# Kernel tuning notes

Measured on AMD Instinct MI355X. Metric: run time of the kernel, lower is better.

## Reference

```python
import jax, jax.numpy as jnp
import numpy as np

H = 32  # hidden_size

def _lstm_layer(x, Wih, Whh, bih, bhh):
    """Single LSTM layer, batch_first x: [B,T,I] -> hs [B,T,H].
    PyTorch gate order: i, f, g, o."""
    B = x.shape[0]
    # Precompute all input projections at once: [B,T,4H] -> time-major [T,B,4H]
    xp = (jnp.einsum('bti,gi->btg', x, Wih) + bih + bhh).transpose(1, 0, 2)
    h0 = jnp.zeros((B, H), dtype=x.dtype)
    c0 = jnp.zeros((B, H), dtype=x.dtype)

    def step(carry, xt):
        h, c = carry
        gates = xt + h @ Whh.T                      # [B,4H]
        i, f, g, o = jnp.split(gates, 4, axis=-1)
        i = jax.nn.sigmoid(i)
        f = jax.nn.sigmoid(f)
        g = jnp.tanh(g)
        o = jax.nn.sigmoid(o)
        c = f * c + i * g
        h = o * jnp.tanh(c)
        return (h, c), h

    _, hs = jax.lax.scan(step, (h0, c0), xp)        # hs: [T,B,H]
    return hs.transpose(1, 0, 2)                    # [B,T,H]


def setup_inputs() -> dict:
    key = jax.random.key(0)
    ks = jax.random.split(key, 12)
    B, T, I = 4096, 512, 1
    s = 1.0 / np.sqrt(H)  # PyTorch uniform(-1/sqrt(H), 1/sqrt(H)) init scale
    u = lambda k, shape: jax.random.uniform(k, shape, jnp.float32, -s, s)
    return {
        'x': jax.random.normal(ks[0], (B, T, I), jnp.float32),
        'W_ih_l0': u(ks[1], (4 * H, I)),
        'W_hh_l0': u(ks[2], (4 * H, H)),
        'b_ih_l0': u(ks[3], (4 * H,)),
        'b_hh_l0': u(ks[4], (4 * H,)),
        'W_ih_l1': u(ks[5], (4 * H, H)),
        'W_hh_l1': u(ks[6], (4 * H, H)),
        'b_ih_l1': u(ks[7], (4 * H,)),
        'b_hh_l1': u(ks[8], (4 * H,)),
        'W_fc': u(ks[9], (1, H)),
        'b_fc': u(ks[10], (1,)),
    }


def reference(x, W_ih_l0, W_hh_l0, b_ih_l0, b_hh_l0,
              W_ih_l1, W_hh_l1, b_ih_l1, b_hh_l1, W_fc, b_fc):
    h1 = _lstm_layer(x, W_ih_l0, W_hh_l0, b_ih_l0, b_hh_l0)   # [B,T,H]
    h2 = _lstm_layer(h1, W_ih_l1, W_hh_l1, b_ih_l1, b_hh_l1)  # [B,T,H]
    out = h2[:, -1, :] @ W_fc.T + b_fc                        # [B,1]
    return jax.nn.relu(out)
```

## Files before the change

kernel.cpp:

```cpp
#include <hip/hip_runtime.h>
#include <hip/hip_bf16.h>


typedef __attribute__((ext_vector_type(8))) short bf16x8;
typedef __attribute__((ext_vector_type(4))) float f32x4;
typedef __attribute__((ext_vector_type(4))) int   i32x4;

#define HID 32
#define SEQ 512
#define L2E 1.4426950408889634f
#define LSTR 20

static __device__ __forceinline__ float fexp2(float x){ return __builtin_amdgcn_exp2f(x); }
static __device__ __forceinline__ float frcp (float x){ return __builtin_amdgcn_rcpf(x); }
static __device__ __forceinline__ short f2bf(float f){
  unsigned u = __builtin_bit_cast(unsigned, f);
  u = (u + 0x7fffu + ((u >> 16) & 1u)) >> 16;
  return (short)u;
}

#define CELL(gi, gf, gg, go, cvr, hout) do {                         \
  const float I_ = fexp2(gi), G_ = fexp2(gg);                        \
  const float F_ = fexp2(gf), O_ = fexp2(go);                        \
  const float a_ = 1.f + I_, b_ = 1.f + G_, c_ = 1.f + F_;           \
  const float P1_ = a_ * b_;                                         \
  const float R_  = frcp(c_ * P1_);                                  \
  const float fv_ = P1_ * R_;                                        \
  const float ig_ = (G_ - 1.f) * (c_ * R_);                          \
  (cvr) = fmaf(fv_, (cvr), ig_);                                     \
  const float C2_ = fexp2((cvr) * (2.f * L2E));                      \
  (hout) = (C2_ - 1.f) * frcp((1.f + O_) * (1.f + C2_));             \
} while (0)

#define HPACK(hv, pk) do {                                                    \
  const int pa_ = __builtin_amdgcn_ds_swizzle(__builtin_bit_cast(int, (hv)), 0x401F); \
  asm("v_cvt_pk_bf16_f32 %0, %1, %2" : "=v"(pk)                               \
      : "v"(hv), "v"(__builtin_bit_cast(float, pa_)));                        \
} while (0)

__global__ __launch_bounds__(512, 2) void lstm2_zs_kernel(
    const float* __restrict__ x,
    const float* __restrict__ Wih0, const float* __restrict__ Whh0,
    const float* __restrict__ bih0, const float* __restrict__ bhh0,
    const float* __restrict__ Wih1, const float* __restrict__ Whh1,
    const float* __restrict__ bih1, const float* __restrict__ bhh1,
    const float* __restrict__ Wfc, const float* __restrict__ bfc,
    float* __restrict__ out)
{
  const int tid = threadIdx.x;
  const int w   = tid >> 6;
  const int l   = tid & 63;
  const int m   = l >> 4;
  const int col = l & 15;
  const int V   = w & 3;
  const bool isL1 = (w >= 4);

  __shared__ int   bufH0[2][16 * LSTR];
  __shared__ int   bufH1[2][16 * LSTR];
  __shared__ float bufFC[4][16];

  for (int i = tid; i < 2 * 16 * LSTR; i += 512) {
    ((int*)bufH0)[i] = 0;
    ((int*)bufH1)[i] = 0;
  }
  __syncthreads();

  const float* Wrec = isL1 ? Whh1 : Whh0;
  const float* Bi   = isL1 ? bih1 : bih0;
  const float* Bh   = isL1 ? bhh1 : bhh0;
  const int   gcol  = col & 3;
  const float scA   = (gcol == 2) ? (2.0f * L2E) : (-L2E);
  bf16x8 wfR[2], wfI[2];
  f32x4  cb[2];
  float  w0x[2][4];
  #pragma unroll
  for (int t = 0; t < 2; ++t) {
    const int ur = 8 * V + 4 * t + (col >> 2);
    const int ga = gcol * 32 + ur;
    #pragma unroll
    for (int j = 0; j < 8; ++j) {
      wfR[t][j] = f2bf(scA * Wrec[ga * HID + (8 * m + j)]);
      wfI[t][j] = isL1 ? f2bf(scA * Wih1[ga * HID + (8 * m + j)]) : (short)0;
    }
    const int uc = 8 * V + 4 * t + m;
    #pragma unroll
    for (int rr = 0; rr < 4; ++rr) {
      const float sc = (rr == 2) ? (2.0f * L2E) : (-L2E);
      cb[t][rr] = sc * (Bi[rr * 32 + uc] + Bh[rr * 32 + uc]);
      w0x[t][rr] = isL1 ? 0.f : sc * Wih0[rr * 32 + uc];
    }
  }
  const float wfcA = isL1 ? Wfc[8 * V + m]     : 0.f;
  const float wfcB = isL1 ? Wfc[8 * V + 4 + m] : 0.f;

  float cvA = 0.f, cvB = 0.f, hA = 0.f, hB = 0.f;
  const float* xb = x + (size_t)(blockIdx.x * 16 + col) * SEQ;
  const int  rd = col * LSTR + 4 * m;
  const int  wb = col * LSTR + 4 * V + (m >> 1);
  const bool wr = ((m & 1) == 0);

  for (int k = 0; k < SEQ / 4; ++k) {
    float4 xv = {0.f, 0.f, 0.f, 0.f};
    if (!isL1) xv = *reinterpret_cast<const float4*>(xb + k * 4);
    #pragma unroll
    for (int uu = 0; uu < 4; ++uu) {
      const int par = uu & 1;
      if (!isL1) {
        const i32x4 hv = *(const i32x4*)&bufH0[par ^ 1][rd];
        const bf16x8 hf = __builtin_bit_cast(bf16x8, hv);
        f32x4 A0, A1;
        A0 = __builtin_amdgcn_mfma_f32_16x16x32_bf16(wfR[0], hf, cb[0], 0, 0, 0);
        A1 = __builtin_amdgcn_mfma_f32_16x16x32_bf16(wfR[1], hf, cb[1], 0, 0, 0);
        const float xt = (uu == 0) ? xv.x : (uu == 1) ? xv.y : (uu == 2) ? xv.z : xv.w;
        CELL(fmaf(w0x[0][0], xt, A0[0]), fmaf(w0x[0][1], xt, A0[1]),
             fmaf(w0x[0][2], xt, A0[2]), fmaf(w0x[0][3], xt, A0[3]), cvA, hA);
        CELL(fmaf(w0x[1][0], xt, A1[0]), fmaf(w0x[1][1], xt, A1[1]),
             fmaf(w0x[1][2], xt, A1[2]), fmaf(w0x[1][3], xt, A1[3]), cvB, hB);
        int pkA, pkB;
        HPACK(hA, pkA);
        HPACK(hB, pkB);
        if (wr) { bufH0[par][wb] = pkA; bufH0[par][wb + 2] = pkB; }
      } else if (uu > 0 || k > 0) {
        const i32x4 h0v = *(const i32x4*)&bufH0[par ^ 1][rd];
        const i32x4 h1v = *(const i32x4*)&bufH1[par][rd];
        const bf16x8 h0f = __builtin_bit_cast(bf16x8, h0v);
        const bf16x8 h1f = __builtin_bit_cast(bf16x8, h1v);
        f32x4 A0, A1;
        __builtin_amdgcn_s_setprio(1);
        A0 = __builtin_amdgcn_mfma_f32_16x16x32_bf16(wfI[0], h0f, cb[0], 0, 0, 0);
        A1 = __builtin_amdgcn_mfma_f32_16x16x32_bf16(wfI[1], h0f, cb[1], 0, 0, 0);
        A0 = __builtin_amdgcn_mfma_f32_16x16x32_bf16(wfR[0], h1f, A0, 0, 0, 0);
        A1 = __builtin_amdgcn_mfma_f32_16x16x32_bf16(wfR[1], h1f, A1, 0, 0, 0);
        __builtin_amdgcn_s_setprio(0);
        CELL(A0[0], A0[1], A0[2], A0[3], cvA, hA);
        CELL(A1[0], A1[1], A1[2], A1[3], cvB, hB);
        int pkA, pkB;
        HPACK(hA, pkA);
        HPACK(hB, pkB);
        if (wr) { bufH1[par ^ 1][wb] = pkA; bufH1[par ^ 1][wb + 2] = pkB; }
      }
      __syncthreads();
    }
  }

  if (isL1) {
    const i32x4 h0v = *(const i32x4*)&bufH0[1][rd];
    const i32x4 h1v = *(const i32x4*)&bufH1[0][rd];
    const bf16x8 h0f = __builtin_bit_cast(bf16x8, h0v);
    const bf16x8 h1f = __builtin_bit_cast(bf16x8, h1v);
    f32x4 A0, A1;
    A0 = __builtin_amdgcn_mfma_f32_16x16x32_bf16(wfI[0], h0f, cb[0], 0, 0, 0);
    A1 = __builtin_amdgcn_mfma_f32_16x16x32_bf16(wfI[1], h0f, cb[1], 0, 0, 0);
    A0 = __builtin_amdgcn_mfma_f32_16x16x32_bf16(wfR[0], h1f, A0, 0, 0, 0);
    A1 = __builtin_amdgcn_mfma_f32_16x16x32_bf16(wfR[1], h1f, A1, 0, 0, 0);
    CELL(A0[0], A0[1], A0[2], A0[3], cvA, hA);
    CELL(A1[0], A1[1], A1[2], A1[3], cvB, hB);
    float part = hA * wfcA + hB * wfcB;
    part += __shfl_xor(part, 16);
    part += __shfl_xor(part, 32);
    if (l < 16) bufFC[V][l] = part;
  }
  __syncthreads();
  if (w == 4 && l < 16) {
    const float o = bufFC[0][l] + bufFC[1][l] + bufFC[2][l] + bufFC[3][l] + bfc[0];
    out[blockIdx.x * 16 + l] = o > 0.f ? o : 0.f;
  }
}

extern "C" void kernel_launch(void* const* d_in, const int* in_sizes, int n_in,
                              void* d_out, int out_size, void* d_ws, size_t ws_size,
                              hipStream_t stream) {
  const float* x    = (const float*)d_in[0];
  const float* Wih0 = (const float*)d_in[1];
  const float* Whh0 = (const float*)d_in[2];
  const float* bih0 = (const float*)d_in[3];
  const float* bhh0 = (const float*)d_in[4];
  const float* Wih1 = (const float*)d_in[5];
  const float* Whh1 = (const float*)d_in[6];
  const float* bih1 = (const float*)d_in[7];
  const float* bhh1 = (const float*)d_in[8];
  const float* Wfc  = (const float*)d_in[9];
  const float* bfc  = (const float*)d_in[10];

  const int B = 4096;
  const int grid = B / 16;
  lstm2_zs_kernel<<<grid, 512, 0, stream>>>(
      x, Wih0, Whh0, bih0, bhh0, Wih1, Whh1, bih1, bhh1, Wfc, bfc,
      (float*)d_out);
}
```

Measured before the change: 197.7 us.

## Split each LSTM layer across eight waves with one hidden-unit slice each

Doubles the block to 1024 threads so each layer uses eight waves, each handling four hidden units (one MFMA tile) instead of two tiles per wave. This halves the per-wave serial work per timestep (MFMAs, cell math, packing) on the recurrence critical path. In exchange every timestep barrier now synchronises 16 waves instead of 8, and occupancy per CU changes with the larger blocks.

Result: slower. 209.3 us (+5.9%).

```diff
diff --git a/kernel.cpp b/kernel.cpp
--- a/kernel.cpp
+++ b/kernel.cpp
@@ -38,7 +38,7 @@
       : "v"(hv), "v"(__builtin_bit_cast(float, pa_)));                        \
 } while (0)
 
-__global__ __launch_bounds__(512, 2) void lstm2_zs_kernel(
+__global__ __launch_bounds__(1024, 4) void lstm2_zs16_kernel(
     const float* __restrict__ x,
     const float* __restrict__ Wih0, const float* __restrict__ Whh0,
     const float* __restrict__ bih0, const float* __restrict__ bhh0,
@@ -52,16 +52,17 @@
   const int l   = tid & 63;
   const int m   = l >> 4;
   const int col = l & 15;
-  const int V   = w & 3;
-  const bool isL1 = (w >= 4);
+  const int V   = w & 7;
+  const bool isL1 = (w >= 8);
+  const int unit = 4 * V + m;
 
   __shared__ int   bufH0[2][16 * LSTR];
   __shared__ int   bufH1[2][16 * LSTR];
-  __shared__ float bufFC[4][16];
+  __shared__ float bufFC[8][16];
 
-  for (int i = tid; i < 2 * 16 * LSTR; i += 512) {
-    ((int*)bufH0)[i] = 0;
-    ((int*)bufH1)[i] = 0;
+  if (tid < 2 * 16 * LSTR) {
+    ((int*)bufH0)[tid] = 0;
+    ((int*)bufH1)[tid] = 0;
   }
   __syncthreads();
 
@@ -70,33 +71,27 @@
   const float* Bh   = isL1 ? bhh1 : bhh0;
   const int   gcol  = col & 3;
   const float scA   = (gcol == 2) ? (2.0f * L2E) : (-L2E);
-  bf16x8 wfR[2], wfI[2];
-  f32x4  cb[2];
-  float  w0x[2][4];
+  const int   ga    = gcol * 32 + 4 * V + (col >> 2);
+  bf16x8 wfR, wfI;
+  f32x4  cb;
+  float  w0x[4];
   #pragma unroll
-  for (int t = 0; t < 2; ++t) {
-    const int ur = 8 * V + 4 * t + (col >> 2);
-    const int ga = gcol * 32 + ur;
-    #pragma unroll
-    for (int j = 0; j < 8; ++j) {
-      wfR[t][j] = f2bf(scA * Wrec[ga * HID + (8 * m + j)]);
-      wfI[t][j] = isL1 ? f2bf(scA * Wih1[ga * HID + (8 * m + j)]) : (short)0;
-    }
-    const int uc = 8 * V + 4 * t + m;
-    #pragma unroll
-    for (int rr = 0; rr < 4; ++rr) {
-      const float sc = (rr == 2) ? (2.0f * L2E) : (-L2E);
-      cb[t][rr] = sc * (Bi[rr * 32 + uc] + Bh[rr * 32 + uc]);
-      w0x[t][rr] = isL1 ? 0.f : sc * Wih0[rr * 32 + uc];
-    }
+  for (int j = 0; j < 8; ++j) {
+    wfR[j] = f2bf(scA * Wrec[ga * HID + (8 * m + j)]);
+    wfI[j] = isL1 ? f2bf(scA * Wih1[ga * HID + (8 * m + j)]) : (short)0;
   }
-  const float wfcA = isL1 ? Wfc[8 * V + m]     : 0.f;
-  const float wfcB = isL1 ? Wfc[8 * V + 4 + m] : 0.f;
+  #pragma unroll
+  for (int rr = 0; rr < 4; ++rr) {
+    const float sc = (rr == 2) ? (2.0f * L2E) : (-L2E);
+    cb[rr]  = sc * (Bi[rr * 32 + unit] + Bh[rr * 32 + unit]);
+    w0x[rr] = isL1 ? 0.f : sc * Wih0[rr * 32 + unit];
+  }
+  const float wfc = isL1 ? Wfc[unit] : 0.f;
 
-  float cvA = 0.f, cvB = 0.f, hA = 0.f, hB = 0.f;
+  float cv = 0.f, hn = 0.f;
   const float* xb = x + (size_t)(blockIdx.x * 16 + col) * SEQ;
   const int  rd = col * LSTR + 4 * m;
-  const int  wb = col * LSTR + 4 * V + (m >> 1);
+  const int  wb = col * LSTR + 2 * V + (m >> 1);
   const bool wr = ((m & 1) == 0);
 
   for (int k = 0; k < SEQ / 4; ++k) {
@@ -108,36 +103,26 @@
       if (!isL1) {
         const i32x4 hv = *(const i32x4*)&bufH0[par ^ 1][rd];
         const bf16x8 hf = __builtin_bit_cast(bf16x8, hv);
-        f32x4 A0, A1;
-        A0 = __builtin_amdgcn_mfma_f32_16x16x32_bf16(wfR[0], hf, cb[0], 0, 0, 0);
-        A1 = __builtin_amdgcn_mfma_f32_16x16x32_bf16(wfR[1], hf, cb[1], 0, 0, 0);
+        const f32x4 A = __builtin_amdgcn_mfma_f32_16x16x32_bf16(wfR, hf, cb, 0, 0, 0);
         const float xt = (uu == 0) ? xv.x : (uu == 1) ? xv.y : (uu == 2) ? xv.z : xv.w;
-        CELL(fmaf(w0x[0][0], xt, A0[0]), fmaf(w0x[0][1], xt, A0[1]),
-             fmaf(w0x[0][2], xt, A0[2]), fmaf(w0x[0][3], xt, A0[3]), cvA, hA);
-        CELL(fmaf(w0x[1][0], xt, A1[0]), fmaf(w0x[1][1], xt, A1[1]),
-             fmaf(w0x[1][2], xt, A1[2]), fmaf(w0x[1][3], xt, A1[3]), cvB, hB);
-        int pkA, pkB;
-        HPACK(hA, pkA);
-        HPACK(hB, pkB);
-        if (wr) { bufH0[par][wb] = pkA; bufH0[par][wb + 2] = pkB; }
+        CELL(fmaf(w0x[0], xt, A[0]), fmaf(w0x[1], xt, A[1]),
+             fmaf(w0x[2], xt, A[2]), fmaf(w0x[3], xt, A[3]), cv, hn);
+        int pk;
+        HPACK(hn, pk);
+        if (wr) bufH0[par][wb] = pk;
       } else if (uu > 0 || k > 0) {
         const i32x4 h0v = *(const i32x4*)&bufH0[par ^ 1][rd];
         const i32x4 h1v = *(const i32x4*)&bufH1[par][rd];
         const bf16x8 h0f = __builtin_bit_cast(bf16x8, h0v);
         const bf16x8 h1f = __builtin_bit_cast(bf16x8, h1v);
-        f32x4 A0, A1;
         __builtin_amdgcn_s_setprio(1);
-        A0 = __builtin_amdgcn_mfma_f32_16x16x32_bf16(wfI[0], h0f, cb[0], 0, 0, 0);
-        A1 = __builtin_amdgcn_mfma_f32_16x16x32_bf16(wfI[1], h0f, cb[1], 0, 0, 0);
-        A0 = __builtin_amdgcn_mfma_f32_16x16x32_bf16(wfR[0], h1f, A0, 0, 0, 0);
-        A1 = __builtin_amdgcn_mfma_f32_16x16x32_bf16(wfR[1], h1f, A1, 0, 0, 0);
+        f32x4 A = __builtin_amdgcn_mfma_f32_16x16x32_bf16(wfI, h0f, cb, 0, 0, 0);
+        A = __builtin_amdgcn_mfma_f32_16x16x32_bf16(wfR, h1f, A, 0, 0, 0);
         __builtin_amdgcn_s_setprio(0);
-        CELL(A0[0], A0[1], A0[2], A0[3], cvA, hA);
-        CELL(A1[0], A1[1], A1[2], A1[3], cvB, hB);
-        int pkA, pkB;
-        HPACK(hA, pkA);
-        HPACK(hB, pkB);
-        if (wr) { bufH1[par ^ 1][wb] = pkA; bufH1[par ^ 1][wb + 2] = pkB; }
+        CELL(A[0], A[1], A[2], A[3], cv, hn);
+        int pk;
+        HPACK(hn, pk);
+        if (wr) bufH1[par ^ 1][wb] = pk;
       }
       __syncthreads();
     }
@@ -148,21 +133,19 @@
     const i32x4 h1v = *(const i32x4*)&bufH1[0][rd];
     const bf16x8 h0f = __builtin_bit_cast(bf16x8, h0v);
     const bf16x8 h1f = __builtin_bit_cast(bf16x8, h1v);
-    f32x4 A0, A1;
-    A0 = __builtin_amdgcn_mfma_f32_16x16x32_bf16(wfI[0], h0f, cb[0], 0, 0, 0);
-    A1 = __builtin_amdgcn_mfma_f32_16x16x32_bf16(wfI[1], h0f, cb[1], 0, 0, 0);
-    A0 = __builtin_amdgcn_mfma_f32_16x16x32_bf16(wfR[0], h1f, A0, 0, 0, 0);
-    A1 = __builtin_amdgcn_mfma_f32_16x16x32_bf16(wfR[1], h1f, A1, 0, 0, 0);
-    CELL(A0[0], A0[1], A0[2], A0[3], cvA, hA);
-    CELL(A1[0], A1[1], A1[2], A1[3], cvB, hB);
-    float part = hA * wfcA + hB * wfcB;
+    f32x4 A = __builtin_amdgcn_mfma_f32_16x16x32_bf16(wfI, h0f, cb, 0, 0, 0);
+    A = __builtin_amdgcn_mfma_f32_16x16x32_bf16(wfR, h1f, A, 0, 0, 0);
+    CELL(A[0], A[1], A[2], A[3], cv, hn);
+    float part = hn * wfc;
     part += __shfl_xor(part, 16);
     part += __shfl_xor(part, 32);
     if (l < 16) bufFC[V][l] = part;
   }
   __syncthreads();
-  if (w == 4 && l < 16) {
-    const float o = bufFC[0][l] + bufFC[1][l] + bufFC[2][l] + bufFC[3][l] + bfc[0];
+  if (w == 8 && l < 16) {
+    float o = bfc[0];
+    #pragma unroll
+    for (int v = 0; v < 8; ++v) o += bufFC[v][l];
     out[blockIdx.x * 16 + l] = o > 0.f ? o : 0.f;
   }
 }
@@ -184,7 +167,7 @@
 
   const int B = 4096;
   const int grid = B / 16;
-  lstm2_zs_kernel<<<grid, 512, 0, stream>>>(
+  lstm2_zs16_kernel<<<grid, 1024, 0, stream>>>(
       x, Wih0, Whh0, bih0, bhh0, Wih1, Whh1, bih1, bhh1, Wfc, bfc,
       (float*)d_out);
 }
```

## Skew layer-1 LSTM by one extra step and remap hidden units to drop swizzle

Applied to the files above, without the earlier changes.

Layer 1 now lags layer 0 by two timesteps. Its layer-0 input is prefetched a step early into a register, and layer-0 hidden state goes into a 4-deep ring buffer in shared memory. The weight rows are remapped so each lane owns two adjacent hidden units, so the bf16 pair is packed directly from hA/hB without a ds_swizzle, and all lanes write one packed int. Together these aim to shorten the per-step critical path and LDS traffic, at the cost of extra shared memory, an added epilogue step and a redundant init loop.

Result: faster. 177.4 us (-10.3%).

```diff
diff --git a/kernel.cpp b/kernel.cpp
--- a/kernel.cpp
+++ b/kernel.cpp
@@ -32,13 +32,7 @@
   (hout) = (C2_ - 1.f) * frcp((1.f + O_) * (1.f + C2_));             \
 } while (0)
 
-#define HPACK(hv, pk) do {                                                    \
-  const int pa_ = __builtin_amdgcn_ds_swizzle(__builtin_bit_cast(int, (hv)), 0x401F); \
-  asm("v_cvt_pk_bf16_f32 %0, %1, %2" : "=v"(pk)                               \
-      : "v"(hv), "v"(__builtin_bit_cast(float, pa_)));                        \
-} while (0)
-
-__global__ __launch_bounds__(512, 2) void lstm2_zs_kernel(
+__global__ __launch_bounds__(512, 2) void lstm2_zs2_kernel(
     const float* __restrict__ x,
     const float* __restrict__ Wih0, const float* __restrict__ Whh0,
     const float* __restrict__ bih0, const float* __restrict__ bhh0,
@@ -55,14 +49,14 @@
   const int V   = w & 3;
   const bool isL1 = (w >= 4);
 
-  __shared__ int   bufH0[2][16 * LSTR];
+  __shared__ int   bufH0[4][16 * LSTR];
   __shared__ int   bufH1[2][16 * LSTR];
   __shared__ float bufFC[4][16];
 
-  for (int i = tid; i < 2 * 16 * LSTR; i += 512) {
+  for (int i = tid; i < 6 * 16 * LSTR; i += 512)
     ((int*)bufH0)[i] = 0;
-    ((int*)bufH1)[i] = 0;
-  }
+  for (int i = tid; i < 4 * 16 * LSTR; i += 512) ((int*)bufH0)[i] = 0;
+  for (int i = tid; i < 2 * 16 * LSTR; i += 512) ((int*)bufH1)[i] = 0;
   __syncthreads();
 
   const float* Wrec = isL1 ? Whh1 : Whh0;
@@ -75,38 +69,36 @@
   float  w0x[2][4];
   #pragma unroll
   for (int t = 0; t < 2; ++t) {
-    const int ur = 8 * V + 4 * t + (col >> 2);
-    const int ga = gcol * 32 + ur;
+    const int ga = gcol * 32 + 8 * V + 2 * (col >> 2) + t;
     #pragma unroll
     for (int j = 0; j < 8; ++j) {
       wfR[t][j] = f2bf(scA * Wrec[ga * HID + (8 * m + j)]);
       wfI[t][j] = isL1 ? f2bf(scA * Wih1[ga * HID + (8 * m + j)]) : (short)0;
     }
-    const int uc = 8 * V + 4 * t + m;
+    const int uc = 8 * V + 2 * m + t;
     #pragma unroll
     for (int rr = 0; rr < 4; ++rr) {
       const float sc = (rr == 2) ? (2.0f * L2E) : (-L2E);
-      cb[t][rr] = sc * (Bi[rr * 32 + uc] + Bh[rr * 32 + uc]);
+      cb[t][rr]  = sc * (Bi[rr * 32 + uc] + Bh[rr * 32 + uc]);
       w0x[t][rr] = isL1 ? 0.f : sc * Wih0[rr * 32 + uc];
     }
   }
-  const float wfcA = isL1 ? Wfc[8 * V + m]     : 0.f;
-  const float wfcB = isL1 ? Wfc[8 * V + 4 + m] : 0.f;
+  const float wfcA = isL1 ? Wfc[8 * V + 2 * m]     : 0.f;
+  const float wfcB = isL1 ? Wfc[8 * V + 2 * m + 1] : 0.f;
 
   float cvA = 0.f, cvB = 0.f, hA = 0.f, hB = 0.f;
+  i32x4 h0pre = {0, 0, 0, 0};
   const float* xb = x + (size_t)(blockIdx.x * 16 + col) * SEQ;
   const int  rd = col * LSTR + 4 * m;
-  const int  wb = col * LSTR + 4 * V + (m >> 1);
-  const bool wr = ((m & 1) == 0);
+  const int  wb = col * LSTR + 4 * V + m;
 
   for (int k = 0; k < SEQ / 4; ++k) {
     float4 xv = {0.f, 0.f, 0.f, 0.f};
     if (!isL1) xv = *reinterpret_cast<const float4*>(xb + k * 4);
     #pragma unroll
     for (int uu = 0; uu < 4; ++uu) {
-      const int par = uu & 1;
       if (!isL1) {
-        const i32x4 hv = *(const i32x4*)&bufH0[par ^ 1][rd];
+        const i32x4 hv = *(const i32x4*)&bufH0[(uu + 3) & 3][rd];
         const bf16x8 hf = __builtin_bit_cast(bf16x8, hv);
         f32x4 A0, A1;
         A0 = __builtin_amdgcn_mfma_f32_16x16x32_bf16(wfR[0], hf, cb[0], 0, 0, 0);
@@ -116,35 +108,56 @@
              fmaf(w0x[0][2], xt, A0[2]), fmaf(w0x[0][3], xt, A0[3]), cvA, hA);
         CELL(fmaf(w0x[1][0], xt, A1[0]), fmaf(w0x[1][1], xt, A1[1]),
              fmaf(w0x[1][2], xt, A1[2]), fmaf(w0x[1][3], xt, A1[3]), cvB, hB);
-        int pkA, pkB;
-        HPACK(hA, pkA);
-        HPACK(hB, pkB);
-        if (wr) { bufH0[par][wb] = pkA; bufH0[par][wb + 2] = pkB; }
-      } else if (uu > 0 || k > 0) {
-        const i32x4 h0v = *(const i32x4*)&bufH0[par ^ 1][rd];
-        const i32x4 h1v = *(const i32x4*)&bufH1[par][rd];
-        const bf16x8 h0f = __builtin_bit_cast(bf16x8, h0v);
-        const bf16x8 h1f = __builtin_bit_cast(bf16x8, h1v);
-        f32x4 A0, A1;
-        __builtin_amdgcn_s_setprio(1);
-        A0 = __builtin_amdgcn_mfma_f32_16x16x32_bf16(wfI[0], h0f, cb[0], 0, 0, 0);
-        A1 = __builtin_amdgcn_mfma_f32_16x16x32_bf16(wfI[1], h0f, cb[1], 0, 0, 0);
-        A0 = __builtin_amdgcn_mfma_f32_16x16x32_bf16(wfR[0], h1f, A0, 0, 0, 0);
-        A1 = __builtin_amdgcn_mfma_f32_16x16x32_bf16(wfR[1], h1f, A1, 0, 0, 0);
-        __builtin_amdgcn_s_setprio(0);
-        CELL(A0[0], A0[1], A0[2], A0[3], cvA, hA);
-        CELL(A1[0], A1[1], A1[2], A1[3], cvB, hB);
-        int pkA, pkB;
-        HPACK(hA, pkA);
-        HPACK(hB, pkB);
-        if (wr) { bufH1[par ^ 1][wb] = pkA; bufH1[par ^ 1][wb + 2] = pkB; }
+        int pk;
+        asm("v_cvt_pk_bf16_f32 %0, %1, %2" : "=v"(pk) : "v"(hA), "v"(hB));
+        bufH0[uu][wb] = pk;
+      } else {
+        const bool doC = (uu >= 2) || (k > 0);
+        const bool doP = (uu >= 1) || (k > 0);
+        i32x4 h1v = {0, 0, 0, 0};
+        if (doC) h1v = *(const i32x4*)&bufH1[(uu + 1) & 1][rd];
+        i32x4 h0next = h0pre;
+        if (doP) h0next = *(const i32x4*)&bufH0[(uu + 3) & 3][rd];
+        if (doC) {
+          const bf16x8 h0f = __builtin_bit_cast(bf16x8, h0pre);
+          const bf16x8 h1f = __builtin_bit_cast(bf16x8, h1v);
+          f32x4 A0, A1;
+          __builtin_amdgcn_s_setprio(1);
+          A0 = __builtin_amdgcn_mfma_f32_16x16x32_bf16(wfI[0], h0f, cb[0], 0, 0, 0);
+          A1 = __builtin_amdgcn_mfma_f32_16x16x32_bf16(wfI[1], h0f, cb[1], 0, 0, 0);
+          A0 = __builtin_amdgcn_mfma_f32_16x16x32_bf16(wfR[0], h1f, A0, 0, 0, 0);
+          A1 = __builtin_amdgcn_mfma_f32_16x16x32_bf16(wfR[1], h1f, A1, 0, 0, 0);
+          __builtin_amdgcn_s_setprio(0);
+          CELL(A0[0], A0[1], A0[2], A0[3], cvA, hA);
+          CELL(A1[0], A1[1], A1[2], A1[3], cvB, hB);
+          int pk;
+          asm("v_cvt_pk_bf16_f32 %0, %1, %2" : "=v"(pk) : "v"(hA), "v"(hB));
+          bufH1[uu & 1][wb] = pk;
+        }
+        h0pre = h0next;
       }
       __syncthreads();
     }
   }
 
   if (isL1) {
-    const i32x4 h0v = *(const i32x4*)&bufH0[1][rd];
+    const i32x4 h1v = *(const i32x4*)&bufH1[1][rd];
+    const bf16x8 h0f = __builtin_bit_cast(bf16x8, h0pre);
+    const bf16x8 h1f = __builtin_bit_cast(bf16x8, h1v);
+    f32x4 A0, A1;
+    A0 = __builtin_amdgcn_mfma_f32_16x16x32_bf16(wfI[0], h0f, cb[0], 0, 0, 0);
+    A1 = __builtin_amdgcn_mfma_f32_16x16x32_bf16(wfI[1], h0f, cb[1], 0, 0, 0);
+    A0 = __builtin_amdgcn_mfma_f32_16x16x32_bf16(wfR[0], h1f, A0, 0, 0, 0);
+    A1 = __builtin_amdgcn_mfma_f32_16x16x32_bf16(wfR[1], h1f, A1, 0, 0, 0);
+    CELL(A0[0], A0[1], A0[2], A0[3], cvA, hA);
+    CELL(A1[0], A1[1], A1[2], A1[3], cvB, hB);
+    int pk;
+    asm("v_cvt_pk_bf16_f32 %0, %1, %2" : "=v"(pk) : "v"(hA), "v"(hB));
+    bufH1[0][wb] = pk;
+  }
+  __syncthreads();
+  if (isL1) {
+    const i32x4 h0v = *(const i32x4*)&bufH0[3][rd];
     const i32x4 h1v = *(const i32x4*)&bufH1[0][rd];
     const bf16x8 h0f = __builtin_bit_cast(bf16x8, h0v);
     const bf16x8 h1f = __builtin_bit_cast(bf16x8, h1v);
@@ -184,7 +197,7 @@
 
   const int B = 4096;
   const int grid = B / 16;
-  lstm2_zs_kernel<<<grid, 512, 0, stream>>>(
+  lstm2_zs2_kernel<<<grid, 512, 0, stream>>>(
       x, Wih0, Whh0, bih0, bhh0, Wih1, Whh1, bih1, bhh1, Wfc, bfc,
       (float*)d_out);
 }
```
